# Kernel optimization log

Hardware: AMD Instinct MI355X
Metric: run time of the kernel (lower is better)

## Reference

```python
import jax, jax.numpy as jnp
import numpy as np

B, T, D = 2, 2048, 1024
H, HD = 16, 64           # num_heads, head_dim (key_dim = value_dim = H*HD = D)
K = 4                    # short conv kernel size
EPS = 1e-6


def setup_inputs() -> dict:
    key = jax.random.key(0)
    ks = jax.random.split(key, 16)
    w = lambda k, shape, s=0.02: jax.random.normal(k, shape, jnp.float32) * s
    dt = jnp.exp(jax.random.uniform(ks[12], (H,)) * (np.log(0.1) - np.log(0.001)) + np.log(0.001))
    dt = jnp.clip(dt, 0.0001, None)
    return {
        "hidden_states": jax.random.normal(ks[0], (B, T, D), jnp.float32),
        "Wq": w(ks[1], (H * HD, D)),
        "Wk": w(ks[2], (H * HD, D)),
        "Wv": w(ks[3], (H * HD, D)),
        "Wa": w(ks[4], (H, D)),
        "Wb": w(ks[5], (H, D)),
        "Wg": w(ks[6], (H * HD, D)),
        "Wo": w(ks[7], (D, H * HD)),
        "q_norm_w": jnp.ones((HD,), jnp.float32),
        "k_norm_w": jnp.ones((HD,), jnp.float32),
        "o_norm_w": jnp.ones((HD,), jnp.float32),
        "A_log": jnp.log(jax.random.uniform(ks[11], (H,), jnp.float32, 0.5, 8.0)),
        "dt_bias": dt + jnp.log(-jnp.expm1(-dt)),
        "conv_q_w": w(ks[13], (H * HD, K), 0.2),
        "conv_k_w": w(ks[14], (H * HD, K), 0.2),
        "conv_v_w": w(ks[15], (H * HD, K), 0.2),
    }


def _short_conv_silu(x, w):
    # causal depthwise conv1d (kernel K) + SiLU; x: [B,T,C], w: [C,K]
    xc = jnp.transpose(x, (0, 2, 1))                       # [B,C,T]
    y = jax.lax.conv_general_dilated(
        xc, w[:, None, :], (1,), [(w.shape[-1] - 1, 0)],
        dimension_numbers=("NCH", "OIH", "NCH"), feature_group_count=w.shape[0])
    y = jnp.transpose(y, (0, 2, 1))
    return y * jax.nn.sigmoid(y)


def _rmsnorm(x, w):
    return x * jax.lax.rsqrt(jnp.mean(x * x, -1, keepdims=True) + EPS) * w


def _l2norm(x):
    return x * jax.lax.rsqrt(jnp.sum(x * x, -1, keepdims=True) + EPS)


def _forward(hidden_states, Wq, Wk, Wv, Wa, Wb, Wg, Wo,
             q_norm_w, k_norm_w, o_norm_w, A_log, dt_bias,
             conv_q_w, conv_k_w, conv_v_w):
    h = hidden_states
    q = _short_conv_silu(h @ Wq.T, conv_q_w).reshape(B, T, H, HD)
    k = _short_conv_silu(h @ Wk.T, conv_k_w).reshape(B, T, H, HD)
    v = _short_conv_silu(h @ Wv.T, conv_v_w).reshape(B, T, H, HD)
    q = _l2norm(_rmsnorm(q, q_norm_w))
    k = _l2norm(_rmsnorm(k, k_norm_w))
    beta = jax.nn.sigmoid(h @ Wb.T)                                  # [B,T,H]
    g = -jnp.exp(A_log) * jax.nn.softplus(h @ Wa.T + dt_bias)        # [B,T,H]
    scale = HD ** -0.5

    def step(S, inp):  # S: [B,H,dk,dv]
        qt, kt, vt, gt, bt = inp
        S = S * jnp.exp(gt)[:, :, None, None]
        kv = jnp.einsum("bhk,bhkv->bhv", kt, S)
        delta = (vt - kv) * bt[..., None]
        S = S + jnp.einsum("bhk,bhv->bhkv", kt, delta)
        o = jnp.einsum("bhk,bhkv->bhv", qt * scale, S)
        return S, o

    tm = lambda x: jnp.swapaxes(x, 0, 1)  # [B,T,...] -> [T,B,...]
    S0 = jnp.zeros((B, H, HD, HD), jnp.float32)
    _, o = jax.lax.scan(step, S0, (tm(q), tm(k), tm(v), tm(g), tm(beta)))
    o = jnp.swapaxes(o, 0, 1)                                        # [B,T,H,HD]

    gv = (h @ Wg.T).reshape(B, T, H, HD)
    o = _rmsnorm(o, o_norm_w) * (gv * jax.nn.sigmoid(gv))            # swish gate
    return o.reshape(B, T, H * HD) @ Wo.T


def reference(hidden_states, Wq, Wk, Wv, Wa, Wb, Wg, Wo,
              q_norm_w, k_norm_w, o_norm_w, A_log, dt_bias,
              conv_q_w, conv_k_w, conv_v_w):
    return _forward(hidden_states, Wq, Wk, Wv, Wa, Wb, Wg, Wo,
                    q_norm_w, k_norm_w, o_norm_w, A_log, dt_bias,
                    conv_q_w, conv_k_w, conv_v_w)
```

## Files before the change

### kernel.cpp

```cpp
#include <hip/hip_runtime.h>
#include <cstdint>
#include <cstddef>

#define B_ 2
#define T_ 2048
#define D_ 1024
#define H_ 16
#define HD_ 64
#define NC_ 32

typedef unsigned short u16;
typedef __attribute__((ext_vector_type(8))) short bf16x8;
typedef __attribute__((ext_vector_type(4))) float f32x4;

__device__ __forceinline__ float dot4(float4 a, float4 b, float acc) {
  return fmaf(a.x, b.x, fmaf(a.y, b.y, fmaf(a.z, b.z, fmaf(a.w, b.w, acc))));
}
__device__ __forceinline__ u16 f2bf(float f) {
  unsigned u = __float_as_uint(f);
  u += 0x7fffu + ((u >> 16) & 1u);
  return (u16)(u >> 16);
}
__device__ __forceinline__ float bf2f(u16 v) {
  return __uint_as_float(((unsigned)v) << 16);
}
__device__ __forceinline__ float4 ld4bf(const u16* p) {
  uint2 v = *(const uint2*)p;
  return float4{__uint_as_float(v.x << 16),
                __uint_as_float(v.x & 0xffff0000u),
                __uint_as_float(v.y << 16),
                __uint_as_float(v.y & 0xffff0000u)};
}
__device__ __forceinline__ bf16x8 pack8(float4 a, float4 b) {
  union { u16 us[8]; bf16x8 v; } p;
  p.us[0] = f2bf(a.x); p.us[1] = f2bf(a.y); p.us[2] = f2bf(a.z); p.us[3] = f2bf(a.w);
  p.us[4] = f2bf(b.x); p.us[5] = f2bf(b.y); p.us[6] = f2bf(b.z); p.us[7] = f2bf(b.w);
  return p.v;
}
__device__ __forceinline__ void glds16(const u16* g, u16* l) {
  __builtin_amdgcn_global_load_lds(
      (const __attribute__((address_space(1))) void*)g,
      (__attribute__((address_space(3))) void*)l, 16, 0, 0);
}
__device__ __forceinline__ float4 conv4(float4 x0, float4 x1, float4 x2, float4 x3,
                                        const float4* w) {
  float4 y;
  y.x = fmaf(w[0].x, x0.x, fmaf(w[0].y, x1.x, fmaf(w[0].z, x2.x, w[0].w * x3.x)));
  y.y = fmaf(w[1].x, x0.y, fmaf(w[1].y, x1.y, fmaf(w[1].z, x2.y, w[1].w * x3.y)));
  y.z = fmaf(w[2].x, x0.z, fmaf(w[2].y, x1.z, fmaf(w[2].z, x2.z, w[2].w * x3.z)));
  y.w = fmaf(w[3].x, x0.w, fmaf(w[3].y, x1.w, fmaf(w[3].z, x2.w, w[3].w * x3.w)));
  return y;
}
__device__ __forceinline__ float4 silu4(float4 a) {
  return float4{a.x / (1.f + __expf(-a.x)), a.y / (1.f + __expf(-a.y)),
                a.z / (1.f + __expf(-a.z)), a.w / (1.f + __expf(-a.w))};
}

__global__ __launch_bounds__(256) void cvt_all(
    const float* __restrict__ h, const float* __restrict__ w0,
    const float* __restrict__ w1, const float* __restrict__ w2,
    const float* __restrict__ w3, const float* __restrict__ w4,
    u16* __restrict__ h_bf, u16* __restrict__ wb)
{
  const int blk = blockIdx.x;
  const float* src;
  u16* dst;
  int lb;
  if (blk < 2048) { src = h; dst = h_bf; lb = blk; }
  else {
    int k = (blk - 2048) >> 9, r = (blk - 2048) & 511;
    src = k == 0 ? w0 : k == 1 ? w1 : k == 2 ? w2 : k == 3 ? w3 : w4;
    dst = wb + (size_t)k * 1048576;
    lb = r;
  }
  int i = (lb * 256 + threadIdx.x) * 8;
  float4 v0 = *(const float4*)(src + i);
  float4 v1 = *(const float4*)(src + i + 4);
  union { u16 us[8]; uint4 u4; } p;
  p.us[0] = f2bf(v0.x); p.us[1] = f2bf(v0.y); p.us[2] = f2bf(v0.z); p.us[3] = f2bf(v0.w);
  p.us[4] = f2bf(v1.x); p.us[5] = f2bf(v1.y); p.us[6] = f2bf(v1.z); p.us[7] = f2bf(v1.w);
  *(uint4*)(dst + i) = p.u4;
}

__device__ __forceinline__ void gemm_core256bf(const u16* __restrict__ A,
    const u16* __restrict__ Bw, u16* __restrict__ C,
    u16* As, u16* Bs, int row0, int col0, int K, int N)
{
  const int tid = threadIdx.x;
  const int lane = tid & 63, wave = tid >> 6;
  const int wr = (wave >> 1) * 128, wc = (wave & 1) * 64;
  const int lr = lane & 15, lkq = lane >> 4;
  const int lkp = (lkq ^ ((lr >> 1) & 3)) * 8;
  const int rql = (lane >> 2);
  const int cql = (((lane & 3) ^ ((rql >> 1) & 3))) * 8;
  const u16* gA[4];
  const u16* gB[2];
  #pragma unroll
  for (int i = 0; i < 4; ++i)
    gA[i] = A + (size_t)(row0 + (wave + 4*i) * 16 + rql) * K + cql;
  #pragma unroll
  for (int j = 0; j < 2; ++j)
    gB[j] = Bw + (size_t)(col0 + (wave + 4*j) * 16 + rql) * K + cql;

  f32x4 acc[8][4];
  #pragma unroll
  for (int i = 0; i < 8; ++i)
    #pragma unroll
    for (int j = 0; j < 4; ++j) acc[i][j] = f32x4{0.f, 0.f, 0.f, 0.f};

  auto STAGE = [&](int buf, int kt) {
    u16* ab = As + buf * 8192;
    u16* bb = Bs + buf * 4096;
    #pragma unroll
    for (int i = 0; i < 4; ++i) glds16(gA[i] + kt * 32, ab + (wave + 4*i) * 512);
    #pragma unroll
    for (int j = 0; j < 2; ++j) glds16(gB[j] + kt * 32, bb + (wave + 4*j) * 512);
  };

  const int KT = K >> 5;
  STAGE(0, 0);
  STAGE(1, 1);
  int cur = 0;
  for (int kt = 0; kt < KT; ++kt) {
    if (kt + 2 < KT) {
      STAGE(cur == 0 ? 2 : (cur == 1 ? 0 : 1), kt + 2);
      asm volatile("s_waitcnt vmcnt(12)" ::: "memory");
    } else if (kt + 1 < KT) {
      asm volatile("s_waitcnt vmcnt(6)" ::: "memory");
    } else {
      asm volatile("s_waitcnt vmcnt(0)" ::: "memory");
    }
    __builtin_amdgcn_s_barrier();
    __builtin_amdgcn_sched_barrier(0);
    const u16* Asc = As + cur * 8192;
    const u16* Bsc = Bs + cur * 4096;
    bf16x8 af[8], bf[4];
    #pragma unroll
    for (int i = 0; i < 8; ++i) af[i] = *(const bf16x8*)&Asc[(wr + i * 16 + lr) * 32 + lkp];
    #pragma unroll
    for (int j = 0; j < 4; ++j) bf[j] = *(const bf16x8*)&Bsc[(wc + j * 16 + lr) * 32 + lkp];
    #pragma unroll
    for (int i = 0; i < 8; ++i)
      #pragma unroll
      for (int j = 0; j < 4; ++j)
        acc[i][j] = __builtin_amdgcn_mfma_f32_16x16x32_bf16(af[i], bf[j], acc[i][j], 0, 0, 0);
    __builtin_amdgcn_sched_barrier(0);
    __builtin_amdgcn_s_barrier();
    cur = (cur == 2) ? 0 : cur + 1;
  }
  const int orow = row0 + wr + lkq * 4;
  const int ocol = col0 + wc + lr;
  #pragma unroll
  for (int i = 0; i < 8; ++i)
    #pragma unroll
    for (int j = 0; j < 4; ++j)
      #pragma unroll
      for (int r = 0; r < 4; ++r)
        C[(size_t)(orow + i * 16 + r) * N + ocol + j * 16] = f2bf(acc[i][j][r]);
}

__device__ __forceinline__ void gemm_core128(const u16* __restrict__ A,
    const u16* __restrict__ Bw, float* __restrict__ C,
    u16* As, u16* Bs, int row0, int col0, int K, int N)
{
  const int tid = threadIdx.x;
  const int lane = tid & 63, wave = tid >> 6;
  const int wr = (wave >> 1) * 64, wc = (wave & 1) * 64;
  const int lr = lane & 15;
  const int lkp = (((lane >> 4) ^ ((lr >> 1) & 3))) * 8;
  const int rql = (lane >> 2);
  const int cql = (((lane & 3) ^ ((rql >> 1) & 3))) * 8;
  const u16* gA0 = A + (size_t)(row0 + wave * 16 + rql) * K + cql;
  const u16* gA1 = A + (size_t)(row0 + (wave + 4) * 16 + rql) * K + cql;
  const u16* gB0 = Bw + (size_t)(col0 + wave * 16 + rql) * K + cql;
  const u16* gB1 = Bw + (size_t)(col0 + (wave + 4) * 16 + rql) * K + cql;

  f32x4 acc[4][4];
  #pragma unroll
  for (int i = 0; i < 4; ++i)
    #pragma unroll
    for (int j = 0; j < 4; ++j) acc[i][j] = f32x4{0.f, 0.f, 0.f, 0.f};

  auto STAGE = [&](int buf, int kt) {
    u16* ab = As + buf * 4096;
    u16* bb = Bs + buf * 4096;
    glds16(gA0 + kt * 32, ab + wave * 512);
    glds16(gA1 + kt * 32, ab + (wave + 4) * 512);
    glds16(gB0 + kt * 32, bb + wave * 512);
    glds16(gB1 + kt * 32, bb + (wave + 4) * 512);
  };

  const int KT = K >> 5;
  STAGE(0, 0);
  STAGE(1, 1);
  int cur = 0;
  for (int kt = 0; kt < KT; ++kt) {
    if (kt + 2 < KT) {
      STAGE(cur == 0 ? 2 : (cur == 1 ? 0 : 1), kt + 2);
      asm volatile("s_waitcnt vmcnt(8)" ::: "memory");
    } else if (kt + 1 < KT) {
      asm volatile("s_waitcnt vmcnt(4)" ::: "memory");
    } else {
      asm volatile("s_waitcnt vmcnt(0)" ::: "memory");
    }
    __builtin_amdgcn_s_barrier();
    __builtin_amdgcn_sched_barrier(0);
    const u16* Asc = As + cur * 4096;
    const u16* Bsc = Bs + cur * 4096;
    bf16x8 af[4], bf[4];
    #pragma unroll
    for (int i = 0; i < 4; ++i) af[i] = *(const bf16x8*)&Asc[(wr + i * 16 + lr) * 32 + lkp];
    #pragma unroll
    for (int j = 0; j < 4; ++j) bf[j] = *(const bf16x8*)&Bsc[(wc + j * 16 + lr) * 32 + lkp];
    #pragma unroll
    for (int i = 0; i < 4; ++i)
      #pragma unroll
      for (int j = 0; j < 4; ++j)
        acc[i][j] = __builtin_amdgcn_mfma_f32_16x16x32_bf16(af[i], bf[j], acc[i][j], 0, 0, 0);
    __builtin_amdgcn_sched_barrier(0);
    __builtin_amdgcn_s_barrier();
    cur = (cur == 2) ? 0 : cur + 1;
  }
  const int orow = row0 + wr + (lane >> 4) * 4;
  const int ocol = col0 + wc + lr;
  #pragma unroll
  for (int i = 0; i < 4; ++i)
    #pragma unroll
    for (int j = 0; j < 4; ++j)
      #pragma unroll
      for (int r = 0; r < 4; ++r)
        C[(size_t)(orow + i * 16 + r) * N + ocol + j * 16] = acc[i][j][r];
}

__global__ __launch_bounds__(256) void gemm_bf16_4(const u16* __restrict__ A,
    const u16* __restrict__ W0, const u16* __restrict__ W1,
    const u16* __restrict__ W2, const u16* __restrict__ W3,
    u16* __restrict__ C0, u16* __restrict__ C1,
    u16* __restrict__ C2, u16* __restrict__ C3)
{
  __shared__ u16 As[3 * 256 * 32];
  __shared__ u16 Bs[3 * 128 * 32];
  const int sel = blockIdx.y >> 3;
  const u16* Bw = sel == 0 ? W0 : sel == 1 ? W1 : sel == 2 ? W2 : W3;
  u16* C = sel == 0 ? C0 : sel == 1 ? C1 : sel == 2 ? C2 : C3;
  gemm_core256bf(A, Bw, C, As, Bs, blockIdx.x * 256, (blockIdx.y & 7) * 128, 1024, 1024);
}

__global__ __launch_bounds__(256) void gemm_bf16_1(const u16* __restrict__ A,
    const u16* __restrict__ Bw, float* __restrict__ C)
{
  __shared__ u16 As[3 * 128 * 32];
  __shared__ u16 Bs[3 * 128 * 32];
  gemm_core128(A, Bw, C, As, Bs, blockIdx.x * 128, blockIdx.y * 128, 1024, 1024);
}

#define SPW 261
__global__ __launch_bounds__(256) void smallproj(const float* __restrict__ Hs,
    const float* __restrict__ Wa, const float* __restrict__ Wb,
    const float* __restrict__ Alog, const float* __restrict__ dtb,
    float* __restrict__ Gout, float* __restrict__ Bout)
{
  __shared__ float hT[16][SPW];
  __shared__ float wT[32][SPW];
  const int row0 = blockIdx.x * 16;
  const int tid = threadIdx.x;
  const int r = tid >> 5;
  const int c = tid & 31;
  float a0 = 0.f, a1 = 0.f;
  for (int kc = 0; kc < 4; ++kc) {
    const int k0 = kc * 256;
    #pragma unroll
    for (int i = 0; i < 4; ++i) {
      int e4 = tid + i * 256;
      int rr = e4 >> 6, k4 = (e4 & 63) * 4;
      *(float4*)&hT[rr][k4] = *(const float4*)&Hs[(size_t)(row0 + rr) * D_ + k0 + k4];
    }
    #pragma unroll
    for (int i = 0; i < 8; ++i) {
      int e4 = tid + i * 256;
      int rr = e4 >> 6, k4 = (e4 & 63) * 4;
      const float* wsrc = (rr < 16) ? (Wa + (size_t)rr * D_) : (Wb + (size_t)(rr - 16) * D_);
      *(float4*)&wT[rr][k4] = *(const float4*)&wsrc[k0 + k4];
    }
    __syncthreads();
    #pragma unroll 8
    for (int k = 0; k < 256; k += 4) {
      float4 wv = *(const float4*)&wT[c][k];
      float4 h0 = *(const float4*)&hT[r][k];
      float4 h1 = *(const float4*)&hT[r + 8][k];
      a0 = dot4(h0, wv, a0);
      a1 = dot4(h1, wv, a1);
    }
    __syncthreads();
  }
  if (c < 16) {
    const float al = -__expf(Alog[c]);
    const float db = dtb[c];
    float x0 = a0 + db, x1 = a1 + db;
    float sp0 = fmaxf(x0, 0.f) + log1pf(__expf(-fabsf(x0)));
    float sp1 = fmaxf(x1, 0.f) + log1pf(__expf(-fabsf(x1)));
    Gout[(size_t)(row0 + r) * H_ + c] = al * sp0;
    Gout[(size_t)(row0 + r + 8) * H_ + c] = al * sp1;
  } else {
    const int hd = c - 16;
    Bout[(size_t)(row0 + r) * H_ + hd] = 1.f / (1.f + __expf(-a0));
    Bout[(size_t)(row0 + r + 8) * H_ + hd] = 1.f / (1.f + __expf(-a1));
  }
}

__global__ __launch_bounds__(256) void p1_chunk(
    const u16* __restrict__ Kp, const u16* __restrict__ Vp,
    const float* __restrict__ Gg, const float* __restrict__ Bb,
    const float* __restrict__ ckw, const float* __restrict__ cvw,
    const float* __restrict__ knw,
    u16* __restrict__ Ubf, u16* __restrict__ Wbf, u16* __restrict__ Kcb,
    float* __restrict__ Gcum, float* __restrict__ Mbuf, float* __restrict__ Nbuf)
{
  __shared__ u16 Kbf[64][72];
  __shared__ float Am[64][68];
  __shared__ float XT[128][68];
  __shared__ float gc[64], bet[64];
  const int bhc = blockIdx.x;
  const int bh = bhc >> 5, c = bhc & 31;
  const int b = bh >> 4, h = bh & 15;
  const int tid = threadIdx.x;
  const int lane = tid & 63, wave = tid >> 6;
  const int lr = lane & 15, lkq = lane >> 4;
  const size_t rowbase = ((size_t)b*T_ + c*64)*H_ + h;
  const int c4 = (tid & 15) * 4;
  const int hh64 = h * 64;

  if (tid < 64) {
    float gv = Gg[rowbase + (size_t)tid*H_];
    #pragma unroll
    for (int off = 1; off < 64; off <<= 1) {
      float up = __shfl_up(gv, off, 64);
      if (tid >= off) gv += up;
    }
    gc[tid] = gv;
    Gcum[(size_t)bhc*64 + tid] = gv;
    bet[tid] = Bb[rowbase + (size_t)tid*H_];
  }

  {
    float4 wk[4];
    float nwv[4];
    #pragma unroll
    for (int cc = 0; cc < 4; ++cc) {
      wk[cc] = *(const float4*)(ckw + (hh64 + c4 + cc) * 4);
      nwv[cc] = knw[c4 + cc];
    }
    #pragma unroll
    for (int k = 0; k < 4; ++k) {
      const int t = (tid >> 4) + k * 16;
      const int gt = c * 64 + t;
      const u16* src = Kp + (rowbase + (size_t)t * H_) * 64 + c4;
      float4 x3 = ld4bf(src);
      float4 x2 = (gt >= 1) ? ld4bf(src - D_)   : float4{0,0,0,0};
      float4 x1 = (gt >= 2) ? ld4bf(src - 2*D_) : float4{0,0,0,0};
      float4 x0 = (gt >= 3) ? ld4bf(src - 3*D_) : float4{0,0,0,0};
      float4 y = silu4(conv4(x0, x1, x2, x3, wk));
      float ss = fmaf(y.x, y.x, fmaf(y.y, y.y, fmaf(y.z, y.z, y.w * y.w)));
      ss += __shfl_xor(ss, 1); ss += __shfl_xor(ss, 2);
      ss += __shfl_xor(ss, 4); ss += __shfl_xor(ss, 8);
      const float inv1 = rsqrtf(ss * (1.f/64.f) + 1e-6f);
      float4 z = {y.x*inv1*nwv[0], y.y*inv1*nwv[1], y.z*inv1*nwv[2], y.w*inv1*nwv[3]};
      float s2 = fmaf(z.x, z.x, fmaf(z.y, z.y, fmaf(z.z, z.z, z.w * z.w)));
      s2 += __shfl_xor(s2, 1); s2 += __shfl_xor(s2, 2);
      s2 += __shfl_xor(s2, 4); s2 += __shfl_xor(s2, 8);
      const float inv2 = rsqrtf(s2 + 1e-6f);
      u16 tmp[4] = {f2bf(z.x*inv2), f2bf(z.y*inv2), f2bf(z.z*inv2), f2bf(z.w*inv2)};
      *(uint2*)&Kbf[t][c4] = *(uint2*)tmp;
      *(uint2*)&Kcb[(size_t)bhc*4096 + (size_t)t*64 + c4] = *(uint2*)tmp;
    }
  }
  __syncthreads();

  {
    bf16x8 afA[2];
    #pragma unroll
    for (int ks = 0; ks < 2; ++ks)
      afA[ks] = *(const bf16x8*)&Kbf[16*wave + lr][ks*32 + lkq*8];
    #pragma unroll
    for (int j = 0; j < 4; ++j) {
      f32x4 accA = f32x4{0.f, 0.f, 0.f, 0.f};
      #pragma unroll
      for (int ks = 0; ks < 2; ++ks) {
        bf16x8 bfr = *(const bf16x8*)&Kbf[16*j + lr][ks*32 + lkq*8];
        accA = __builtin_amdgcn_mfma_f32_16x16x32_bf16(afA[ks], bfr, accA, 0, 0, 0);
      }
      const int s = 16*j + lr;
      #pragma unroll
      for (int r = 0; r < 4; ++r) {
        int t = 16*wave + lkq*4 + r;
        Am[t][s] = (s < t) ? bet[t] * __expf(gc[t] - gc[s]) * accA[r] : 0.f;
      }
    }
  }
  {
    float4 wv[4];
    #pragma unroll
    for (int cc = 0; cc < 4; ++cc)
      wv[cc] = *(const float4*)(cvw + (hh64 + c4 + cc) * 4);
    #pragma unroll
    for (int k = 0; k < 4; ++k) {
      const int t = (tid >> 4) + k * 16;
      const int gt = c * 64 + t;
      const u16* src = Vp + (rowbase + (size_t)t * H_) * 64 + c4;
      float4 x3 = ld4bf(src);
      float4 x2 = (gt >= 1) ? ld4bf(src - D_)   : float4{0,0,0,0};
      float4 x1 = (gt >= 2) ? ld4bf(src - 2*D_) : float4{0,0,0,0};
      float4 x0 = (gt >= 3) ? ld4bf(src - 3*D_) : float4{0,0,0,0};
      float4 vv = silu4(conv4(x0, x1, x2, x3, wv));
      const float bt = bet[t];
      const float ek = bt * __expf(gc[t]);
      XT[c4+0][t] = bt * vv.x; XT[c4+1][t] = bt * vv.y;
      XT[c4+2][t] = bt * vv.z; XT[c4+3][t] = bt * vv.w;
      XT[64+c4+0][t] = ek * bf2f(Kbf[t][c4+0]);
      XT[64+c4+1][t] = ek * bf2f(Kbf[t][c4+1]);
      XT[64+c4+2][t] = ek * bf2f(Kbf[t][c4+2]);
      XT[64+c4+3][t] = ek * bf2f(Kbf[t][c4+3]);
    }
  }
  __syncthreads();

  for (int st = 0; st < 4; ++st) {
    if (st > 0) {
      const int nks = (st == 3) ? 2 : 1;
      f32x4 accU0 = f32x4{0.f,0.f,0.f,0.f}, accU1 = f32x4{0.f,0.f,0.f,0.f};
      for (int ks = 0; ks < nks; ++ks) {
        const int m0 = ks*32 + lkq*8;
        bf16x8 af;
        if (m0 + 8 <= 16*st) {
          float4 a0 = *(const float4*)&Am[16*st + lr][m0];
          float4 a1 = *(const float4*)&Am[16*st + lr][m0 + 4];
          af = pack8(a0, a1);
        } else {
          af = bf16x8{0,0,0,0,0,0,0,0};
        }
        {
          const int cb = (wave*2 + 0) * 16;
          float4 b0 = *(const float4*)&XT[cb + lr][m0];
          float4 b1 = *(const float4*)&XT[cb + lr][m0 + 4];
          accU0 = __builtin_amdgcn_mfma_f32_16x16x32_bf16(af, pack8(b0, b1), accU0, 0, 0, 0);
        }
        {
          const int cb = (wave*2 + 1) * 16;
          float4 b0 = *(const float4*)&XT[cb + lr][m0];
          float4 b1 = *(const float4*)&XT[cb + lr][m0 + 4];
          accU1 = __builtin_amdgcn_mfma_f32_16x16x32_bf16(af, pack8(b0, b1), accU1, 0, 0, 0);
        }
      }
      #pragma unroll
      for (int r = 0; r < 4; ++r) {
        const int t = 16*st + lkq*4 + r;
        XT[(wave*2+0)*16 + lr][t] -= accU0[r];
        XT[(wave*2+1)*16 + lr][t] -= accU1[r];
      }
      __syncthreads();
    }
    if (tid < 128) {
      const int bs = 16*st;
      float x[16];
      #pragma unroll
      for (int q = 0; q < 4; ++q)
        *(float4*)&x[q*4] = *(const float4*)&XT[tid][bs + q*4];
      #pragma unroll
      for (int tau = 1; tau < 16; ++tau) {
        float a = 0.f, a2 = 0.f;
        #pragma unroll
        for (int m = 0; m < tau; m += 2) {
          a = fmaf(Am[bs+tau][bs+m], x[m], a);
          if (m + 1 < tau) a2 = fmaf(Am[bs+tau][bs+m+1], x[m+1], a2);
        }
        x[tau] -= (a + a2);
      }
      #pragma unroll
      for (int q = 0; q < 4; ++q)
        *(float4*)&XT[tid][bs + q*4] = *(const float4*)&x[q*4];
    }
    __syncthreads();
  }

  for (int e = tid; e < 4096; e += 256) {
    int t = e >> 6, j = e & 63;
    Ubf[(size_t)bhc*4096 + e] = f2bf(XT[j][t]);
    Wbf[(size_t)bhc*4096 + e] = f2bf(XT[64+j][t]);
  }

  u16* KTb = (u16*)&Am[0][0];
  if (tid < 64) bet[tid] = __expf(gc[63] - gc[tid]);
  __syncthreads();
  for (int e4 = tid; e4 < 1024; e4 += 256) {
    int t = e4 >> 4, a4 = (e4 & 15) * 4;
    u16 k0 = Kbf[t][a4+0], k1 = Kbf[t][a4+1], k2 = Kbf[t][a4+2], k3 = Kbf[t][a4+3];
    KTb[(a4+0)*72 + t] = k0;
    KTb[(a4+1)*72 + t] = k1;
    KTb[(a4+2)*72 + t] = k2;
    KTb[(a4+3)*72 + t] = k3;
  }
  __syncthreads();

  bf16x8 afK[2];
  #pragma unroll
  for (int ks = 0; ks < 2; ++ks)
    afK[ks] = *(const bf16x8*)&KTb[(16*wave + lr)*72 + ks*32 + lkq*8];
  const float bC = __expf(gc[63]);
  const size_t ob = (size_t)bhc * 4096;
  #pragma unroll
  for (int j = 0; j < 4; ++j) {
    f32x4 aM = f32x4{0.f,0.f,0.f,0.f}, aN = f32x4{0.f,0.f,0.f,0.f};
    #pragma unroll
    for (int ks = 0; ks < 2; ++ks) {
      const int m0 = ks*32 + lkq*8;
      float4 sc0 = *(const float4*)&bet[m0];
      float4 sc1 = *(const float4*)&bet[m0 + 4];
      float4 w0 = *(const float4*)&XT[64 + 16*j + lr][m0];
      float4 w1 = *(const float4*)&XT[64 + 16*j + lr][m0 + 4];
      float4 u0 = *(const float4*)&XT[16*j + lr][m0];
      float4 u1 = *(const float4*)&XT[16*j + lr][m0 + 4];
      w0.x*=sc0.x; w0.y*=sc0.y; w0.z*=sc0.z; w0.w*=sc0.w;
      w1.x*=sc1.x; w1.y*=sc1.y; w1.z*=sc1.z; w1.w*=sc1.w;
      u0.x*=sc0.x; u0.y*=sc0.y; u0.z*=sc0.z; u0.w*=sc0.w;
      u1.x*=sc1.x; u1.y*=sc1.y; u1.z*=sc1.z; u1.w*=sc1.w;
      aM = __builtin_amdgcn_mfma_f32_16x16x32_bf16(afK[ks], pack8(w0, w1), aM, 0, 0, 0);
      aN = __builtin_amdgcn_mfma_f32_16x16x32_bf16(afK[ks], pack8(u0, u1), aN, 0, 0, 0);
    }
    const int cc = 16*j + lr;
    #pragma unroll
    for (int r = 0; r < 4; ++r) {
      const int a = 16*wave + lkq*4 + r;
      Mbuf[ob + (size_t)a*64 + cc] = (a == cc ? bC : 0.f) - aM[r];
      Nbuf[ob + (size_t)a*64 + cc] = aN[r];
    }
  }
}

__global__ __launch_bounds__(256) void pscanA(float* __restrict__ Mbuf,
    float* __restrict__ Nbuf)
{
  __shared__ float OM[2][64][68];
  __shared__ float ON[2][64][68];
  __shared__ float NM[2][64][68];
  const int blk = blockIdx.x;
  const int bh = blk >> 3, g = blk & 7;
  const size_t s0 = ((size_t)bh * 32 + g * 4) * 4096;
  const int tid = threadIdx.x;
  const int p0 = (tid >> 4) * 4;
  const int q0 = (tid & 15) * 4;
  for (int e4 = tid; e4 < 1024; e4 += 256) {
    int r = e4 >> 4, c4 = (e4 & 15) * 4;
    *(float4*)&OM[0][r][c4] = *(const float4*)&Mbuf[s0 + (size_t)r*64 + c4];
    *(float4*)&ON[0][r][c4] = *(const float4*)&Nbuf[s0 + (size_t)r*64 + c4];
    *(float4*)&NM[0][r][c4] = *(const float4*)&Mbuf[s0 + 4096 + (size_t)r*64 + c4];
  }
  __syncthreads();
  for (int s = 0; s < 3; ++s) {
    const int cur = s & 1, nxt = cur ^ 1;
    const size_t wslot = s0 + (size_t)(s + 1) * 4096;
    if (s < 2) {
      for (int e4 = tid; e4 < 1024; e4 += 256) {
        int r = e4 >> 4, c4 = (e4 & 15) * 4;
        *(float4*)&NM[nxt][r][c4] = *(const float4*)&Mbuf[wslot + 4096 + (size_t)r*64 + c4];
      }
    }
    float aM[4][4], aN[4][4];
    #pragma unroll
    for (int r = 0; r < 4; ++r) {
      float4 nv = *(const float4*)&Nbuf[wslot + (size_t)(p0+r)*64 + q0];
      aM[r][0]=0.f; aM[r][1]=0.f; aM[r][2]=0.f; aM[r][3]=0.f;
      aN[r][0]=nv.x; aN[r][1]=nv.y; aN[r][2]=nv.z; aN[r][3]=nv.w;
    }
    for (int m4 = 0; m4 < 64; m4 += 4) {
      float xv[4][4];
      #pragma unroll
      for (int r = 0; r < 4; ++r) {
        float4 v = *(const float4*)&NM[cur][p0+r][m4];
        xv[r][0]=v.x; xv[r][1]=v.y; xv[r][2]=v.z; xv[r][3]=v.w;
      }
      #pragma unroll
      for (int mm = 0; mm < 4; ++mm) {
        float4 ym = *(const float4*)&OM[cur][m4+mm][q0];
        float4 yn = *(const float4*)&ON[cur][m4+mm][q0];
        #pragma unroll
        for (int r = 0; r < 4; ++r) {
          aM[r][0] = fmaf(xv[r][mm], ym.x, aM[r][0]);
          aM[r][1] = fmaf(xv[r][mm], ym.y, aM[r][1]);
          aM[r][2] = fmaf(xv[r][mm], ym.z, aM[r][2]);
          aM[r][3] = fmaf(xv[r][mm], ym.w, aM[r][3]);
          aN[r][0] = fmaf(xv[r][mm], yn.x, aN[r][0]);
          aN[r][1] = fmaf(xv[r][mm], yn.y, aN[r][1]);
          aN[r][2] = fmaf(xv[r][mm], yn.z, aN[r][2]);
          aN[r][3] = fmaf(xv[r][mm], yn.w, aN[r][3]);
        }
      }
    }
    #pragma unroll
    for (int r = 0; r < 4; ++r) {
      float4 vm = {aM[r][0], aM[r][1], aM[r][2], aM[r][3]};
      float4 vn = {aN[r][0], aN[r][1], aN[r][2], aN[r][3]};
      *(float4*)&Mbuf[wslot + (size_t)(p0+r)*64 + q0] = vm;
      *(float4*)&Nbuf[wslot + (size_t)(p0+r)*64 + q0] = vn;
      *(float4*)&OM[nxt][p0+r][q0] = vm;
      *(float4*)&ON[nxt][p0+r][q0] = vn;
    }
    __syncthreads();
  }
}

__global__ __launch_bounds__(256) void pscanB(const float* __restrict__ Mbuf,
    const float* __restrict__ Nbuf, float* __restrict__ S0b)
{
  __shared__ float ST[2][64][68];
  __shared__ float MT[64][68];
  const int bh = blockIdx.x;
  const size_t base = (size_t)bh * 32 * 4096;
  const int tid = threadIdx.x;
  const int j0 = (tid >> 4) * 4, a0 = tid & 15;
  for (int e4 = tid; e4 < 1024; e4 += 256) {
    int r = e4 >> 4, c4 = (e4 & 15) * 4;
    *(float4*)&ST[0][r][c4] = float4{0.f, 0.f, 0.f, 0.f};
    *(float4*)&S0b[base + (size_t)r*64 + c4] = float4{0.f, 0.f, 0.f, 0.f};
  }
  for (int g = 0; g < 7; ++g) {
    const int cur = g & 1, nxt = cur ^ 1;
    const size_t tslot = base + (size_t)(4*g + 3) * 4096;
    for (int e4 = tid; e4 < 1024; e4 += 256) {
      int r = e4 >> 4, c4 = (e4 & 15) * 4;
      *(float4*)&MT[r][c4] = *(const float4*)&Mbuf[tslot + (size_t)r*64 + c4];
    }
    float acc[4][4];
    #pragma unroll
    for (int r = 0; r < 4; ++r)
      #pragma unroll
      for (int s = 0; s < 4; ++s)
        acc[r][s] = Nbuf[tslot + (size_t)(a0 + 16*s)*64 + j0 + r];
    __syncthreads();
    for (int k4 = 0; k4 < 64; k4 += 4) {
      float4 xr[4];
      #pragma unroll
      for (int r = 0; r < 4; ++r) xr[r] = *(const float4*)&ST[cur][j0+r][k4];
      #pragma unroll
      for (int s = 0; s < 4; ++s) {
        float4 yv = *(const float4*)&MT[a0 + 16*s][k4];
        #pragma unroll
        for (int r = 0; r < 4; ++r) acc[r][s] = dot4(xr[r], yv, acc[r][s]);
      }
    }
    const size_t oslot = base + (size_t)(4*(g+1)) * 4096;
    #pragma unroll
    for (int r = 0; r < 4; ++r)
      #pragma unroll
      for (int s = 0; s < 4; ++s) {
        ST[nxt][j0+r][a0 + 16*s] = acc[r][s];
        S0b[oslot + (size_t)(j0+r)*64 + a0 + 16*s] = acc[r][s];
      }
    __syncthreads();
  }
}

__global__ __launch_bounds__(256) void pscanC(const float* __restrict__ Mbuf,
    const float* __restrict__ Nbuf, float* __restrict__ S0b)
{
  __shared__ float ST[64][68];
  __shared__ float MT[64][68];
  const int blk = blockIdx.x;
  const int bh = blk / 24, rem = blk % 24;
  const int g = rem / 3, i = rem % 3 + 1;
  const size_t base = (size_t)bh * 32 * 4096;
  const size_t pslot = base + (size_t)(4*g + i - 1) * 4096;
  const int tid = threadIdx.x;
  const int j0 = (tid >> 4) * 4, a0 = tid & 15;
  for (int e4 = tid; e4 < 1024; e4 += 256) {
    int r = e4 >> 4, c4 = (e4 & 15) * 4;
    *(float4*)&ST[r][c4] = *(const float4*)&S0b[base + (size_t)(4*g)*4096 + (size_t)r*64 + c4];
    *(float4*)&MT[r][c4] = *(const float4*)&Mbuf[pslot + (size_t)r*64 + c4];
  }
  float acc[4][4];
  #pragma unroll
  for (int r = 0; r < 4; ++r)
    #pragma unroll
    for (int s = 0; s < 4; ++s)
      acc[r][s] = Nbuf[pslot + (size_t)(a0 + 16*s)*64 + j0 + r];
  __syncthreads();
  for (int k4 = 0; k4 < 64; k4 += 4) {
    float4 xr[4];
    #pragma unroll
    for (int r = 0; r < 4; ++r) xr[r] = *(const float4*)&ST[j0+r][k4];
    #pragma unroll
    for (int s = 0; s < 4; ++s) {
      float4 yv = *(const float4*)&MT[a0 + 16*s][k4];
      #pragma unroll
      for (int r = 0; r < 4; ++r) acc[r][s] = dot4(xr[r], yv, acc[r][s]);
    }
  }
  const size_t oslot = base + (size_t)(4*g + i) * 4096;
  #pragma unroll
  for (int r = 0; r < 4; ++r)
    #pragma unroll
    for (int s = 0; s < 4; ++s)
      S0b[oslot + (size_t)(j0+r)*64 + a0 + 16*s] = acc[r][s];
}

__global__ __launch_bounds__(256) void p3_out(
    const u16* __restrict__ Qp, const u16* __restrict__ Kcb,
    const float* __restrict__ cqw, const float* __restrict__ qnw,
    const float* __restrict__ Gcum, const float* __restrict__ S0b,
    const u16* __restrict__ Ubf, const u16* __restrict__ Wbfg,
    const u16* __restrict__ GV, const float* __restrict__ onw,
    u16* __restrict__ OG)
{
  __shared__ u16 Qbf[64][72];
  __shared__ u16 Kbf[64][72];
  __shared__ u16 S0T[64][72];
  __shared__ u16 Wbf[64][72];
  __shared__ u16 Pbf[64][72];
  __shared__ u16 DsT[64][72];
  __shared__ float gcs[64];
  __shared__ float onws[64];
  const int bhc = blockIdx.x;
  const int bh = bhc >> 5, c = bhc & 31;
  const int b = bh >> 4, h = bh & 15;
  const int tid = threadIdx.x;
  const int lane = tid & 63, wave = tid >> 6;
  const int lr = lane & 15, lkq = lane >> 4;
  const size_t rowbase = ((size_t)b*T_ + c*64)*H_ + h;
  const int c4 = (tid & 15) * 4;
  const int hh64 = h * 64;
  if (tid < 64) { gcs[tid] = Gcum[(size_t)bhc*64 + tid]; onws[tid] = onw[tid]; }

  {
    float4 wq[4];
    float nwv[4];
    #pragma unroll
    for (int cc = 0; cc < 4; ++cc) {
      wq[cc] = *(const float4*)(cqw + (hh64 + c4 + cc) * 4);
      nwv[cc] = qnw[c4 + cc];
    }
    #pragma unroll
    for (int k = 0; k < 4; ++k) {
      const int t = (tid >> 4) + k * 16;
      const int gt = c * 64 + t;
      const u16* src = Qp + (rowbase + (size_t)t * H_) * 64 + c4;
      float4 x3 = ld4bf(src);
      float4 x2 = (gt >= 1) ? ld4bf(src - D_)   : float4{0,0,0,0};
      float4 x1 = (gt >= 2) ? ld4bf(src - 2*D_) : float4{0,0,0,0};
      float4 x0 = (gt >= 3) ? ld4bf(src - 3*D_) : float4{0,0,0,0};
      float4 y = silu4(conv4(x0, x1, x2, x3, wq));
      float ss = fmaf(y.x, y.x, fmaf(y.y, y.y, fmaf(y.z, y.z, y.w * y.w)));
      ss += __shfl_xor(ss, 1); ss += __shfl_xor(ss, 2);
      ss += __shfl_xor(ss, 4); ss += __shfl_xor(ss, 8);
      const float inv1 = rsqrtf(ss * (1.f/64.f) + 1e-6f);
      float4 z = {y.x*inv1*nwv[0], y.y*inv1*nwv[1], y.z*inv1*nwv[2], y.w*inv1*nwv[3]};
      float s2 = fmaf(z.x, z.x, fmaf(z.y, z.y, fmaf(z.z, z.z, z.w * z.w)));
      s2 += __shfl_xor(s2, 1); s2 += __shfl_xor(s2, 2);
      s2 += __shfl_xor(s2, 4); s2 += __shfl_xor(s2, 8);
      const float inv2 = rsqrtf(s2 + 1e-6f) * 0.125f;
      u16 tmp[4] = {f2bf(z.x*inv2), f2bf(z.y*inv2), f2bf(z.z*inv2), f2bf(z.w*inv2)};
      *(uint2*)&Qbf[t][c4] = *(uint2*)tmp;
    }
  }
  for (int e4 = tid; e4 < 1024; e4 += 256) {
    int t = e4 >> 4, d4 = (e4 & 15) * 4;
    float4 sv = *(const float4*)&S0b[(size_t)bhc*4096 + (size_t)t*64 + d4];
    u16 as[4] = {f2bf(sv.x), f2bf(sv.y), f2bf(sv.z), f2bf(sv.w)};
    *(uint2*)&Kbf[t][d4] = *(const uint2*)&Kcb[(size_t)bhc*4096 + (size_t)t*64 + d4];
    *(uint2*)&S0T[t][d4] = *(uint2*)as;
    *(uint2*)&Wbf[t][d4] = *(const uint2*)&Wbfg[(size_t)bhc*4096 + (size_t)t*64 + d4];
  }
  __syncthreads();

  const int trow0 = 16*wave + lkq*4;
  bf16x8 aq[2], aw[2];
  #pragma unroll
  for (int ks = 0; ks < 2; ++ks) {
    aq[ks] = *(const bf16x8*)&Qbf[16*wave + lr][ks*32 + lkq*8];
    aw[ks] = *(const bf16x8*)&Wbf[16*wave + lr][ks*32 + lkq*8];
  }
  float gct[4], egt[4];
  #pragma unroll
  for (int r = 0; r < 4; ++r) { gct[r] = gcs[trow0 + r]; egt[r] = __expf(gct[r]); }

  #pragma unroll
  for (int j = 0; j < 4; ++j) {
    f32x4 pa = f32x4{0.f,0.f,0.f,0.f};
    #pragma unroll
    for (int ks = 0; ks < 2; ++ks) {
      bf16x8 bk = *(const bf16x8*)&Kbf[16*j + lr][ks*32 + lkq*8];
      pa = __builtin_amdgcn_mfma_f32_16x16x32_bf16(aq[ks], bk, pa, 0, 0, 0);
    }
    const int s = 16*j + lr;
    const float gs = gcs[s];
    #pragma unroll
    for (int r = 0; r < 4; ++r) {
      const int t = trow0 + r;
      float val = (s <= t) ? __expf(gct[r] - gs) * pa[r] : 0.f;
      Pbf[t][s] = f2bf(val);
    }
  }

  #pragma unroll
  for (int j = 0; j < 4; ++j) {
    f32x4 da = f32x4{0.f,0.f,0.f,0.f};
    #pragma unroll
    for (int ks = 0; ks < 2; ++ks) {
      bf16x8 bs = *(const bf16x8*)&S0T[16*j + lr][ks*32 + lkq*8];
      da = __builtin_amdgcn_mfma_f32_16x16x32_bf16(aw[ks], bs, da, 0, 0, 0);
    }
    const int jj = 16*j + lr;
    #pragma unroll
    for (int r = 0; r < 4; ++r) {
      const int s = trow0 + r;
      float dv = bf2f(Ubf[(size_t)bhc*4096 + (size_t)s*64 + jj]) - da[r];
      DsT[jj][s] = f2bf(dv);
    }
  }

  f32x4 oacc[4];
  #pragma unroll
  for (int j = 0; j < 4; ++j) {
    f32x4 oa = f32x4{0.f,0.f,0.f,0.f};
    #pragma unroll
    for (int ks = 0; ks < 2; ++ks) {
      bf16x8 bs = *(const bf16x8*)&S0T[16*j + lr][ks*32 + lkq*8];
      oa = __builtin_amdgcn_mfma_f32_16x16x32_bf16(aq[ks], bs, oa, 0, 0, 0);
    }
    #pragma unroll
    for (int r = 0; r < 4; ++r) oa[r] *= egt[r];
    oacc[j] = oa;
  }
  __syncthreads();

  bf16x8 ap[2];
  #pragma unroll
  for (int ks = 0; ks < 2; ++ks)
    ap[ks] = *(const bf16x8*)&Pbf[16*wave + lr][ks*32 + lkq*8];
  #pragma unroll
  for (int j = 0; j < 4; ++j) {
    #pragma unroll
    for (int ks = 0; ks < 2; ++ks) {
      bf16x8 bd = *(const bf16x8*)&DsT[16*j + lr][ks*32 + lkq*8];
      oacc[j] = __builtin_amdgcn_mfma_f32_16x16x32_bf16(ap[ks], bd, oacc[j], 0, 0, 0);
    }
  }

  #pragma unroll
  for (int r = 0; r < 4; ++r) {
    float ss = 0.f;
    #pragma unroll
    for (int jq = 0; jq < 4; ++jq) ss = fmaf(oacc[jq][r], oacc[jq][r], ss);
    ss += __shfl_xor(ss, 1); ss += __shfl_xor(ss, 2);
    ss += __shfl_xor(ss, 4); ss += __shfl_xor(ss, 8);
    const float inv = rsqrtf(ss * (1.f/64.f) + 1e-6f);
    const int t = trow0 + r;
    const size_t rowoff = ((size_t)b*T_ + (size_t)c*64 + t) * D_ + h*64;
    #pragma unroll
    for (int jq = 0; jq < 4; ++jq) {
      const int jj = 16*jq + lr;
      float y = oacc[jq][r] * inv * onws[jj];
      float gv = bf2f(GV[rowoff + jj]);
      OG[rowoff + jj] = f2bf(y * gv / (1.f + __expf(-gv)));
    }
  }
}

extern "C" void kernel_launch(void* const* d_in, const int* in_sizes, int n_in,
                              void* d_out, int out_size, void* d_ws, size_t ws_size,
                              hipStream_t stream) {
  const float* h    = (const float*)d_in[0];
  const float* Wq   = (const float*)d_in[1];
  const float* Wk   = (const float*)d_in[2];
  const float* Wv   = (const float*)d_in[3];
  const float* Wa   = (const float*)d_in[4];
  const float* Wb   = (const float*)d_in[5];
  const float* Wg   = (const float*)d_in[6];
  const float* Wo   = (const float*)d_in[7];
  const float* qnw  = (const float*)d_in[8];
  const float* knw  = (const float*)d_in[9];
  const float* onw  = (const float*)d_in[10];
  const float* Alog = (const float*)d_in[11];
  const float* dtb  = (const float*)d_in[12];
  const float* cqw  = (const float*)d_in[13];
  const float* ckw  = (const float*)d_in[14];
  const float* cvw  = (const float*)d_in[15];
  float* out = (float*)d_out;
  float* ws  = (float*)d_ws;

  const size_t NB = (size_t)B_ * T_ * D_;
  float* qp   = ws;
  float* kp   = ws + 1*NB;
  float* vp   = ws + 2*NB;
  float* gvp  = ws + 3*NB;
  float* qc   = ws + 4*NB;
  float* kc   = ws + 5*NB;
  float* vc   = ws + 6*NB;
  float* mb   = ws + 7*NB;
  float* wbf  = ws + 8*NB;
  float* gb   = ws + 8*NB + 5*524288;
  float* bb   = gb + (size_t)B_*T_*H_;
  float* Gc   = bb + (size_t)B_*T_*H_;

  u16* h_bf  = (u16*)mb;
  u16* og_bf = (u16*)mb;
  u16* w_bf  = (u16*)wbf;
  u16* wq_bf = w_bf + 0*1048576;
  u16* wk_bf = w_bf + 1*1048576;
  u16* wv_bf = w_bf + 2*1048576;
  u16* wg_bf = w_bf + 3*1048576;
  u16* wo_bf = w_bf + 4*1048576;

  u16*   Qpb  = (u16*)qp;
  u16*   Kpb  = (u16*)kp;
  u16*   Vpb  = (u16*)vp;
  u16*   GVb  = (u16*)gvp;
  u16*   Ubf  = (u16*)qc;
  u16*   Wbfp = (u16*)qc + NB;
  u16*   Kcb  = (u16*)kc;
  float* Nbuf = vc;
  float* S0b  = vp;
  float* Mbuf = mb;

  cvt_all<<<4608, 256, 0, stream>>>(h, Wq, Wk, Wv, Wg, Wo, h_bf, w_bf);

  gemm_bf16_4<<<dim3(16, 32), 256, 0, stream>>>(h_bf, wq_bf, wk_bf, wv_bf, wg_bf,
                                                 Qpb, Kpb, Vpb, GVb);
  smallproj<<<256, 256, 0, stream>>>(h, Wa, Wb, Alog, dtb, gb, bb);

  p1_chunk<<<B_*H_*NC_, 256, 0, stream>>>(Kpb, Vpb, gb, bb, ckw, cvw, knw,
                                          Ubf, Wbfp, Kcb, Gc, Mbuf, Nbuf);
  pscanA<<<B_*H_*8, 256, 0, stream>>>(Mbuf, Nbuf);
  pscanB<<<B_*H_, 256, 0, stream>>>(Mbuf, Nbuf, S0b);
  pscanC<<<B_*H_*24, 256, 0, stream>>>(Mbuf, Nbuf, S0b);
  p3_out<<<B_*H_*NC_, 256, 0, stream>>>(Qpb, Kcb, cqw, qnw, Gc, S0b, Ubf, Wbfp,
                                        GVb, onw, og_bf);

  gemm_bf16_1<<<dim3(32, 8), 256, 0, stream>>>(og_bf, wo_bf, out);
}
```

Baseline: 228.5 us.

## Fuse pscanC intra-group state fixup into p3_out and add MFMA setprio hints

Measured after the change: 217.9 us. 1.05x faster.

```diff
diff --git a/kernel.cpp b/kernel.cpp
--- a/kernel.cpp
+++ b/kernel.cpp
@@ -381,6 +381,7 @@
     #pragma unroll
     for (int ks = 0; ks < 2; ++ks)
       afA[ks] = *(const bf16x8*)&Kbf[16*wave + lr][ks*32 + lkq*8];
+    __builtin_amdgcn_s_setprio(1);
     #pragma unroll
     for (int j = 0; j < 4; ++j) {
       f32x4 accA = f32x4{0.f, 0.f, 0.f, 0.f};
@@ -396,6 +397,7 @@
         Am[t][s] = (s < t) ? bet[t] * __expf(gc[t] - gc[s]) * accA[r] : 0.f;
       }
     }
+    __builtin_amdgcn_s_setprio(0);
   }
   {
     float4 wv[4];
@@ -428,6 +430,7 @@
     if (st > 0) {
       const int nks = (st == 3) ? 2 : 1;
       f32x4 accU0 = f32x4{0.f,0.f,0.f,0.f}, accU1 = f32x4{0.f,0.f,0.f,0.f};
+      __builtin_amdgcn_s_setprio(1);
       for (int ks = 0; ks < nks; ++ks) {
         const int m0 = ks*32 + lkq*8;
         bf16x8 af;
@@ -451,6 +454,7 @@
           accU1 = __builtin_amdgcn_mfma_f32_16x16x32_bf16(af, pack8(b0, b1), accU1, 0, 0, 0);
         }
       }
+      __builtin_amdgcn_s_setprio(0);
       #pragma unroll
       for (int r = 0; r < 4; ++r) {
         const int t = 16*st + lkq*4 + r;
@@ -510,6 +514,7 @@
   #pragma unroll
   for (int j = 0; j < 4; ++j) {
     f32x4 aM = f32x4{0.f,0.f,0.f,0.f}, aN = f32x4{0.f,0.f,0.f,0.f};
+    __builtin_amdgcn_s_setprio(1);
     #pragma unroll
     for (int ks = 0; ks < 2; ++ks) {
       const int m0 = ks*32 + lkq*8;
@@ -526,6 +531,7 @@
       aM = __builtin_amdgcn_mfma_f32_16x16x32_bf16(afK[ks], pack8(w0, w1), aM, 0, 0, 0);
       aN = __builtin_amdgcn_mfma_f32_16x16x32_bf16(afK[ks], pack8(u0, u1), aN, 0, 0, 0);
     }
+    __builtin_amdgcn_s_setprio(0);
     const int cc = 16*j + lr;
     #pragma unroll
     for (int r = 0; r < 4; ++r) {
@@ -659,53 +665,11 @@
   }
 }
 
-__global__ __launch_bounds__(256) void pscanC(const float* __restrict__ Mbuf,
-    const float* __restrict__ Nbuf, float* __restrict__ S0b)
-{
-  __shared__ float ST[64][68];
-  __shared__ float MT[64][68];
-  const int blk = blockIdx.x;
-  const int bh = blk / 24, rem = blk % 24;
-  const int g = rem / 3, i = rem % 3 + 1;
-  const size_t base = (size_t)bh * 32 * 4096;
-  const size_t pslot = base + (size_t)(4*g + i - 1) * 4096;
-  const int tid = threadIdx.x;
-  const int j0 = (tid >> 4) * 4, a0 = tid & 15;
-  for (int e4 = tid; e4 < 1024; e4 += 256) {
-    int r = e4 >> 4, c4 = (e4 & 15) * 4;
-    *(float4*)&ST[r][c4] = *(const float4*)&S0b[base + (size_t)(4*g)*4096 + (size_t)r*64 + c4];
-    *(float4*)&MT[r][c4] = *(const float4*)&Mbuf[pslot + (size_t)r*64 + c4];
-  }
-  float acc[4][4];
-  #pragma unroll
-  for (int r = 0; r < 4; ++r)
-    #pragma unroll
-    for (int s = 0; s < 4; ++s)
-      acc[r][s] = Nbuf[pslot + (size_t)(a0 + 16*s)*64 + j0 + r];
-  __syncthreads();
-  for (int k4 = 0; k4 < 64; k4 += 4) {
-    float4 xr[4];
-    #pragma unroll
-    for (int r = 0; r < 4; ++r) xr[r] = *(const float4*)&ST[j0+r][k4];
-    #pragma unroll
-    for (int s = 0; s < 4; ++s) {
-      float4 yv = *(const float4*)&MT[a0 + 16*s][k4];
-      #pragma unroll
-      for (int r = 0; r < 4; ++r) acc[r][s] = dot4(xr[r], yv, acc[r][s]);
-    }
-  }
-  const size_t oslot = base + (size_t)(4*g + i) * 4096;
-  #pragma unroll
-  for (int r = 0; r < 4; ++r)
-    #pragma unroll
-    for (int s = 0; s < 4; ++s)
-      S0b[oslot + (size_t)(j0+r)*64 + a0 + 16*s] = acc[r][s];
-}
-
 __global__ __launch_bounds__(256) void p3_out(
     const u16* __restrict__ Qp, const u16* __restrict__ Kcb,
     const float* __restrict__ cqw, const float* __restrict__ qnw,
     const float* __restrict__ Gcum, const float* __restrict__ S0b,
+    const float* __restrict__ Mbuf, const float* __restrict__ Nbuf,
     const u16* __restrict__ Ubf, const u16* __restrict__ Wbfg,
     const u16* __restrict__ GV, const float* __restrict__ onw,
     u16* __restrict__ OG)
@@ -727,6 +691,7 @@
   const size_t rowbase = ((size_t)b*T_ + c*64)*H_ + h;
   const int c4 = (tid & 15) * 4;
   const int hh64 = h * 64;
+  const int ii = c & 3;
   if (tid < 64) { gcs[tid] = Gcum[(size_t)bhc*64 + tid]; onws[tid] = onw[tid]; }
 
   {
@@ -762,13 +727,57 @@
   }
   for (int e4 = tid; e4 < 1024; e4 += 256) {
     int t = e4 >> 4, d4 = (e4 & 15) * 4;
-    float4 sv = *(const float4*)&S0b[(size_t)bhc*4096 + (size_t)t*64 + d4];
-    u16 as[4] = {f2bf(sv.x), f2bf(sv.y), f2bf(sv.z), f2bf(sv.w)};
     *(uint2*)&Kbf[t][d4] = *(const uint2*)&Kcb[(size_t)bhc*4096 + (size_t)t*64 + d4];
-    *(uint2*)&S0T[t][d4] = *(uint2*)as;
     *(uint2*)&Wbf[t][d4] = *(const uint2*)&Wbfg[(size_t)bhc*4096 + (size_t)t*64 + d4];
   }
+  if (ii == 0) {
+    for (int e4 = tid; e4 < 1024; e4 += 256) {
+      int t = e4 >> 4, d4 = (e4 & 15) * 4;
+      float4 sv = *(const float4*)&S0b[(size_t)bhc*4096 + (size_t)t*64 + d4];
+      u16 as[4] = {f2bf(sv.x), f2bf(sv.y), f2bf(sv.z), f2bf(sv.w)};
+      *(uint2*)&S0T[t][d4] = *(uint2*)as;
+    }
+  } else {
+    const size_t gslot = ((size_t)bh*NC_ + (c & ~3)) * 4096;
+    const size_t pslot = ((size_t)bh*NC_ + c - 1) * 4096;
+    for (int e4 = tid; e4 < 1024; e4 += 256) {
+      int t = e4 >> 4, d4 = (e4 & 15) * 4;
+      float4 sg = *(const float4*)&S0b[gslot + (size_t)t*64 + d4];
+      float4 mp = *(const float4*)&Mbuf[pslot + (size_t)t*64 + d4];
+      u16 a1[4] = {f2bf(sg.x), f2bf(sg.y), f2bf(sg.z), f2bf(sg.w)};
+      u16 a2[4] = {f2bf(mp.x), f2bf(mp.y), f2bf(mp.z), f2bf(mp.w)};
+      *(uint2*)&DsT[t][d4] = *(uint2*)a1;
+      *(uint2*)&Pbf[t][d4] = *(uint2*)a2;
+    }
+  }
   __syncthreads();
+
+  if (ii != 0) {
+    const size_t pslot = ((size_t)bh*NC_ + c - 1) * 4096;
+    bf16x8 ag[2];
+    #pragma unroll
+    for (int ks = 0; ks < 2; ++ks)
+      ag[ks] = *(const bf16x8*)&DsT[16*wave + lr][ks*32 + lkq*8];
+    #pragma unroll
+    for (int ab = 0; ab < 4; ++ab) {
+      f32x4 cin;
+      {
+        float4 nv = *(const float4*)&Nbuf[pslot + (size_t)(16*ab + lr)*64 + 16*wave + lkq*4];
+        cin[0] = nv.x; cin[1] = nv.y; cin[2] = nv.z; cin[3] = nv.w;
+      }
+      __builtin_amdgcn_s_setprio(1);
+      #pragma unroll
+      for (int ks = 0; ks < 2; ++ks) {
+        bf16x8 bm = *(const bf16x8*)&Pbf[16*ab + lr][ks*32 + lkq*8];
+        cin = __builtin_amdgcn_mfma_f32_16x16x32_bf16(ag[ks], bm, cin, 0, 0, 0);
+      }
+      __builtin_amdgcn_s_setprio(0);
+      #pragma unroll
+      for (int r = 0; r < 4; ++r)
+        S0T[16*wave + lkq*4 + r][16*ab + lr] = f2bf(cin[r]);
+    }
+    __syncthreads();
+  }
 
   const int trow0 = 16*wave + lkq*4;
   bf16x8 aq[2], aw[2];
@@ -784,11 +793,13 @@
   #pragma unroll
   for (int j = 0; j < 4; ++j) {
     f32x4 pa = f32x4{0.f,0.f,0.f,0.f};
+    __builtin_amdgcn_s_setprio(1);
     #pragma unroll
     for (int ks = 0; ks < 2; ++ks) {
       bf16x8 bk = *(const bf16x8*)&Kbf[16*j + lr][ks*32 + lkq*8];
       pa = __builtin_amdgcn_mfma_f32_16x16x32_bf16(aq[ks], bk, pa, 0, 0, 0);
     }
+    __builtin_amdgcn_s_setprio(0);
     const int s = 16*j + lr;
     const float gs = gcs[s];
     #pragma unroll
@@ -802,11 +813,13 @@
   #pragma unroll
   for (int j = 0; j < 4; ++j) {
     f32x4 da = f32x4{0.f,0.f,0.f,0.f};
+    __builtin_amdgcn_s_setprio(1);
     #pragma unroll
     for (int ks = 0; ks < 2; ++ks) {
       bf16x8 bs = *(const bf16x8*)&S0T[16*j + lr][ks*32 + lkq*8];
       da = __builtin_amdgcn_mfma_f32_16x16x32_bf16(aw[ks], bs, da, 0, 0, 0);
     }
+    __builtin_amdgcn_s_setprio(0);
     const int jj = 16*j + lr;
     #pragma unroll
     for (int r = 0; r < 4; ++r) {
@@ -820,11 +833,13 @@
   #pragma unroll
   for (int j = 0; j < 4; ++j) {
     f32x4 oa = f32x4{0.f,0.f,0.f,0.f};
+    __builtin_amdgcn_s_setprio(1);
     #pragma unroll
     for (int ks = 0; ks < 2; ++ks) {
       bf16x8 bs = *(const bf16x8*)&S0T[16*j + lr][ks*32 + lkq*8];
       oa = __builtin_amdgcn_mfma_f32_16x16x32_bf16(aq[ks], bs, oa, 0, 0, 0);
     }
+    __builtin_amdgcn_s_setprio(0);
     #pragma unroll
     for (int r = 0; r < 4; ++r) oa[r] *= egt[r];
     oacc[j] = oa;
@@ -835,6 +850,7 @@
   #pragma unroll
   for (int ks = 0; ks < 2; ++ks)
     ap[ks] = *(const bf16x8*)&Pbf[16*wave + lr][ks*32 + lkq*8];
+  __builtin_amdgcn_s_setprio(1);
   #pragma unroll
   for (int j = 0; j < 4; ++j) {
     #pragma unroll
@@ -843,6 +859,7 @@
       oacc[j] = __builtin_amdgcn_mfma_f32_16x16x32_bf16(ap[ks], bd, oacc[j], 0, 0, 0);
     }
   }
+  __builtin_amdgcn_s_setprio(0);
 
   #pragma unroll
   for (int r = 0; r < 4; ++r) {
@@ -901,7 +918,7 @@
   float* Gc   = bb + (size_t)B_*T_*H_;
 
   u16* h_bf  = (u16*)mb;
-  u16* og_bf = (u16*)mb;
+  u16* og_bf = (u16*)kp;
   u16* w_bf  = (u16*)wbf;
   u16* wq_bf = w_bf + 0*1048576;
   u16* wk_bf = w_bf + 1*1048576;
@@ -930,9 +947,8 @@
                                           Ubf, Wbfp, Kcb, Gc, Mbuf, Nbuf);
   pscanA<<<B_*H_*8, 256, 0, stream>>>(Mbuf, Nbuf);
   pscanB<<<B_*H_, 256, 0, stream>>>(Mbuf, Nbuf, S0b);
-  pscanC<<<B_*H_*24, 256, 0, stream>>>(Mbuf, Nbuf, S0b);
-  p3_out<<<B_*H_*NC_, 256, 0, stream>>>(Qpb, Kcb, cqw, qnw, Gc, S0b, Ubf, Wbfp,
-                                        GVb, onw, og_bf);
+  p3_out<<<B_*H_*NC_, 256, 0, stream>>>(Qpb, Kcb, cqw, qnw, Gc, S0b, Mbuf, Nbuf,
+                                        Ubf, Wbfp, GVb, onw, og_bf);
 
   gemm_bf16_1<<<dim3(32, 8), 256, 0, stream>>>(og_bf, wo_bf, out);
 }
```
